# Kernel optimization log

Hardware: AMD Instinct MI355X
Metric: run time of the kernel (lower is better)

The kernel has to match this reference:

```python
import jax, jax.numpy as jnp
import numpy as np

D_MODEL = 1024
NUM_HEADS = 16
D_K = D_MODEL // NUM_HEADS


def setup_inputs() -> dict:
    key = jax.random.key(0)
    ks = jax.random.split(key, 11)
    B, S = 2, 2048
    scale = 1.0 / np.sqrt(D_MODEL)
    inp = {
        "q": jax.random.normal(ks[0], (B, S, D_MODEL), jnp.float32),
        "k": jax.random.normal(ks[1], (B, S, D_MODEL), jnp.float32),
        "v": jax.random.normal(ks[2], (B, S, D_MODEL), jnp.float32),
        "Wq": jax.random.normal(ks[3], (D_MODEL, D_MODEL), jnp.float32) * scale,
        "bq": jnp.zeros((D_MODEL,), jnp.float32),
        "Wk": jax.random.normal(ks[4], (D_MODEL, D_MODEL), jnp.float32) * scale,
        "bk": jnp.zeros((D_MODEL,), jnp.float32),
        "Wv": jax.random.normal(ks[5], (D_MODEL, D_MODEL), jnp.float32) * scale,
        "bv": jnp.zeros((D_MODEL,), jnp.float32),
        "Wo": jax.random.normal(ks[6], (D_MODEL, D_MODEL), jnp.float32) * scale,
        "bo": jnp.zeros((D_MODEL,), jnp.float32),
    }
    return inp


def _split_heads(x):
    B, S, _ = x.shape
    return x.reshape(B, S, NUM_HEADS, D_K).transpose(0, 2, 1, 3)  # [B,H,S,dk]


def reference(q, k, v, Wq, bq, Wk, bk, Wv, bv, Wo, bo):
    Q = _split_heads(q @ Wq.T + bq)  # [B,H,S,dk]
    K = _split_heads(k @ Wk.T + bk)
    V = _split_heads(v @ Wv.T + bv)
    scores = jnp.einsum("bhqd,bhkd->bhqk", Q, K) / jnp.sqrt(jnp.float32(D_K))
    attn = jax.nn.softmax(scores, axis=-1)
    ctx = jnp.einsum("bhqk,bhkd->bhqd", attn, V)  # [B,H,S,dk]
    B, H, S, dk = ctx.shape
    ctx = ctx.transpose(0, 2, 1, 3).reshape(B, S, D_MODEL)
    return ctx @ Wo.T + bo
```

## Files before the change

kernel.cpp:

```cpp
#include <hip/hip_runtime.h>
#include <hip/hip_bf16.h>

typedef unsigned short ushort_t;
typedef __attribute__((ext_vector_type(4))) float f32x4;
typedef __attribute__((ext_vector_type(16))) float f32x16;
typedef __attribute__((ext_vector_type(8))) short short8;
typedef __attribute__((ext_vector_type(4))) unsigned short us4;

#define D_MODEL 1024
#define NHEAD 16
#define DK 64
#define BATCH 2
#define SEQ 2048
#define MTOT 4096
#define EX (MTOT * D_MODEL)
#define EW (D_MODEL * D_MODEL)
#define NROWS (32 * SEQ)

#define MFMA16(a,b,c) __builtin_amdgcn_mfma_f32_16x16x32_bf16((a),(b),(c),0,0,0)
#define MFMA32(a,b,c) __builtin_amdgcn_mfma_f32_32x32x16_bf16((a),(b),(c),0,0,0)

__device__ __forceinline__ ushort_t f2bf(float f){
    union{float f;unsigned u;}c; c.f=f;
    unsigned u=c.u, r=u+0x7FFFu+((u>>16)&1u);
    return (ushort_t)(r>>16);
}
__device__ __forceinline__ unsigned cvtpk_bf(float a, float b){
    float2 t; t.x = a; t.y = b;
    union{ __hip_bfloat162 h; unsigned u; } c;
    c.h = __float22bfloat162_rn(t);
    return c.u;
}
__device__ __forceinline__ void plswap(unsigned &a, unsigned &b){
    asm volatile("v_permlane32_swap_b32 %0, %1" : "+v"(a), "+v"(b));
}
__device__ __forceinline__ void gload16(const ushort_t* g, ushort_t* l){
    __builtin_amdgcn_global_load_lds((const __attribute__((address_space(1))) unsigned*)g,
                                     (__attribute__((address_space(3))) unsigned*)l, 16, 0, 0);
}
__device__ __forceinline__ int xcd_swz(int nwg){
    int s = blockIdx.x;
    return (s & 7) * (nwg >> 3) + (s >> 3);
}

__global__ void cast1(const float* __restrict__ x, ushort_t* __restrict__ y, int n4){
    int i = blockIdx.x*blockDim.x + threadIdx.x, st = gridDim.x*blockDim.x;
    for(; i < n4; i += st){
        f32x4 v = ((const f32x4*)x)[i];
        us4 o; o[0]=f2bf(v[0]); o[1]=f2bf(v[1]); o[2]=f2bf(v[2]); o[3]=f2bf(v[3]);
        ((us4*)y)[i] = o;
    }
}
__global__ void cast4(const float* __restrict__ a, const float* __restrict__ b,
                      const float* __restrict__ c, const float* __restrict__ d4,
                      ushort_t* __restrict__ dst, int n4){
    const float* s = blockIdx.y==0 ? a : (blockIdx.y==1 ? b : (blockIdx.y==2 ? c : d4));
    us4* d = (us4*)(dst + (size_t)blockIdx.y * n4 * 4);
    const f32x4* sv = (const f32x4*)s;
    int i = blockIdx.x*blockDim.x + threadIdx.x, st = gridDim.x*blockDim.x;
    for(; i < n4; i += st){
        f32x4 v = sv[i];
        us4 o; o[0]=f2bf(v[0]); o[1]=f2bf(v[1]); o[2]=f2bf(v[2]); o[3]=f2bf(v[3]);
        d[i] = o;
    }
}

__device__ __forceinline__ void gemm_body(
    const ushort_t* __restrict__ A, const ushort_t* __restrict__ Bm,
    const float* __restrict__ bias, float scale, int bm, int bn, int mode,
    void* __restrict__ out,
    ushort_t* As0, ushort_t* As1, ushort_t* Bs0, ushort_t* Bs1)
{
    const int tid = threadIdx.x, lane = tid & 63, wid = tid >> 6;
    const int row0 = bm << 7, col0 = bn << 7;
    const int wrow = (wid >> 1) << 6, wcol = (wid & 1) << 6;
    const int l4 = lane >> 2, lc = (lane & 3) << 3, lr = lane & 15, ko = (lane >> 4) << 3;
    const f32x4 Z4 = {0.f,0.f,0.f,0.f};

    f32x4 acc[4][4];
#pragma unroll
    for(int i=0;i<4;i++)
#pragma unroll
        for(int j=0;j<4;j++) acc[i][j] = Z4;

#define GSTAGE(AS,BS,k0) do{ \
    gload16(A +(size_t)(row0+32*wid   +l4)*D_MODEL+(k0)+lc, (AS)+(2*wid  )*512); \
    gload16(A +(size_t)(row0+32*wid+16+l4)*D_MODEL+(k0)+lc, (AS)+(2*wid+1)*512); \
    gload16(Bm+(size_t)(col0+32*wid   +l4)*D_MODEL+(k0)+lc, (BS)+(2*wid  )*512); \
    gload16(Bm+(size_t)(col0+32*wid+16+l4)*D_MODEL+(k0)+lc, (BS)+(2*wid+1)*512); \
}while(0)
#define GCOMP(AS,BS) do{ \
    short8 af[4], bf[4]; \
    _Pragma("unroll") for(int i=0;i<4;i++) af[i]=*(const short8*)((AS)+(wrow+i*16+lr)*32+ko); \
    _Pragma("unroll") for(int j=0;j<4;j++) bf[j]=*(const short8*)((BS)+(wcol+j*16+lr)*32+ko); \
    __builtin_amdgcn_s_setprio(1); \
    _Pragma("unroll") for(int i=0;i<4;i++) \
    _Pragma("unroll") for(int j=0;j<4;j++) acc[i][j]=MFMA16(af[i],bf[j],acc[i][j]); \
    __builtin_amdgcn_s_setprio(0); \
}while(0)

    GSTAGE(As0,Bs0,0);
    __syncthreads();
#pragma unroll 1
    for(int t=0; t<32; t+=2){
        if(t+1<32) GSTAGE(As1,Bs1,(t+1)*32);
        GCOMP(As0,Bs0);
        __syncthreads();
        if(t+2<32) GSTAGE(As0,Bs0,(t+2)*32);
        GCOMP(As1,Bs1);
        __syncthreads();
    }
#undef GSTAGE

    const int rr4 = (lane >> 4) << 2;
#pragma unroll
    for(int i=0;i<4;i++){
#pragma unroll
        for(int j=0;j<4;j++){
            const int m0 = row0 + wrow + i*16 + rr4;
            const int n  = col0 + wcol + j*16 + lr;
            const float bs = bias[n];
            if(mode == 2){
                float* O = (float*)out;
#pragma unroll
                for(int r=0;r<4;r++) O[(size_t)(m0+r)*D_MODEL+n] = (acc[i][j][r]+bs)*scale;
            } else if(mode == 0){
                ushort_t* O = (ushort_t*)out;
#pragma unroll
                for(int r=0;r<4;r++) O[(size_t)(m0+r)*D_MODEL+n] = f2bf((acc[i][j][r]+bs)*scale);
            } else {
                ushort_t* O = (ushort_t*)out;
                const int bb = m0 >> 11, s = m0 & 2047, h = n >> 6, d = n & 63;
                us4 p;
#pragma unroll
                for(int r=0;r<4;r++) p[r] = f2bf((acc[i][j][r]+bs)*scale);
                *(us4*)(O + ((size_t)(bb*NHEAD + h)*DK + d)*SEQ + s) = p;
            }
        }
    }
#undef GCOMP
}

#define QSCALE (0.125f * 1.44269504088896f)

__global__ __launch_bounds__(256,2)
void qkv_fused(const float* __restrict__ Xq, const float* __restrict__ Xk,
               const float* __restrict__ Xv,
               const ushort_t* __restrict__ Wq, const ushort_t* __restrict__ Wk,
               const ushort_t* __restrict__ Wv,
               const float* __restrict__ bq, const float* __restrict__ bk,
               const float* __restrict__ bv,
               ushort_t* Qp, ushort_t* Kp, ushort_t* VtG)
{
    __shared__ ushort_t As0[4096], As1[4096], Bs0[4096], Bs1[4096];
    const int wk = xcd_swz(768);
    const int which = wk >> 8, t = wk & 255;
    const float *Af; const ushort_t *Bm; const float* bias; float scale; int mode; void* out;
    if(which == 0){ Af=Xq; Bm=Wq; bias=bq; scale=QSCALE; mode=0; out=Qp; }
    else if(which == 1){ Af=Xk; Bm=Wk; bias=bk; scale=1.f; mode=0; out=Kp; }
    else { Af=Xv; Bm=Wv; bias=bv; scale=1.f; mode=1; out=VtG; }

    const int bm = t >> 3, bn = t & 7;
    const int tid = threadIdx.x, lane = tid & 63, wid = tid >> 6;
    const int row0 = bm << 7, col0 = bn << 7;
    const int wrow = (wid >> 1) << 6, wcol = (wid & 1) << 6;
    const int l4 = lane >> 2, lc = (lane & 3) << 3, lr = lane & 15, ko = (lane >> 4) << 3;
    const f32x4 Z4 = {0.f,0.f,0.f,0.f};

    f32x4 acc[4][4];
#pragma unroll
    for(int i=0;i<4;i++)
#pragma unroll
        for(int j=0;j<4;j++) acc[i][j] = Z4;

    f32x4 ar[2][2][2];

#define ALOAD(R, k0) do{ \
    _Pragma("unroll") for(int c=0;c<2;c++){ \
        const float* src = Af + (size_t)(row0+32*wid+16*c+l4)*D_MODEL + (k0)+lc; \
        (R)[c][0] = *(const f32x4*)(src); \
        (R)[c][1] = *(const f32x4*)(src+4); \
    } \
}while(0)
#define AWRITE(AS, R) do{ \
    _Pragma("unroll") for(int c=0;c<2;c++){ \
        union{ unsigned u[4]; short8 s; } P; \
        P.u[0]=cvtpk_bf((R)[c][0][0],(R)[c][0][1]); \
        P.u[1]=cvtpk_bf((R)[c][0][2],(R)[c][0][3]); \
        P.u[2]=cvtpk_bf((R)[c][1][0],(R)[c][1][1]); \
        P.u[3]=cvtpk_bf((R)[c][1][2],(R)[c][1][3]); \
        *(short8*)((AS) + (2*wid+c)*512 + lane*8) = P.s; \
    } \
}while(0)
#define BSTAGE(BS,k0) do{ \
    gload16(Bm+(size_t)(col0+32*wid   +l4)*D_MODEL+(k0)+lc, (BS)+(2*wid  )*512); \
    gload16(Bm+(size_t)(col0+32*wid+16+l4)*D_MODEL+(k0)+lc, (BS)+(2*wid+1)*512); \
}while(0)
#define GCOMP(AS,BS) do{ \
    short8 af[4], bf[4]; \
    _Pragma("unroll") for(int i=0;i<4;i++) af[i]=*(const short8*)((AS)+(wrow+i*16+lr)*32+ko); \
    _Pragma("unroll") for(int j=0;j<4;j++) bf[j]=*(const short8*)((BS)+(wcol+j*16+lr)*32+ko); \
    __builtin_amdgcn_s_setprio(1); \
    _Pragma("unroll") for(int i=0;i<4;i++) \
    _Pragma("unroll") for(int j=0;j<4;j++) acc[i][j]=MFMA16(af[i],bf[j],acc[i][j]); \
    __builtin_amdgcn_s_setprio(0); \
}while(0)

    ALOAD(ar[0], 0); BSTAGE(Bs0, 0);
    AWRITE(As0, ar[0]);
    __syncthreads();
#pragma unroll 1
    for(int t2=0; t2<32; t2+=2){
        if(t2+1<32){ ALOAD(ar[1], (t2+1)*32); BSTAGE(Bs1, (t2+1)*32); }
        GCOMP(As0,Bs0);
        if(t2+1<32) AWRITE(As1, ar[1]);
        __syncthreads();
        if(t2+2<32){ ALOAD(ar[0], (t2+2)*32); BSTAGE(Bs0, (t2+2)*32); }
        GCOMP(As1,Bs1);
        if(t2+2<32) AWRITE(As0, ar[0]);
        __syncthreads();
    }
#undef ALOAD
#undef AWRITE
#undef BSTAGE
#undef GCOMP

    const int rr4 = (lane >> 4) << 2;
#pragma unroll
    for(int i=0;i<4;i++){
#pragma unroll
        for(int j=0;j<4;j++){
            const int m0 = row0 + wrow + i*16 + rr4;
            const int n  = col0 + wcol + j*16 + lr;
            const float bs = bias[n];
            if(mode == 0){
                ushort_t* O = (ushort_t*)out;
#pragma unroll
                for(int r=0;r<4;r++) O[(size_t)(m0+r)*D_MODEL+n] = f2bf((acc[i][j][r]+bs)*scale);
            } else {
                ushort_t* O = (ushort_t*)out;
                const int bb = m0 >> 11, s = m0 & 2047, h = n >> 6, d = n & 63;
                us4 p;
#pragma unroll
                for(int r=0;r<4;r++) p[r] = f2bf((acc[i][j][r]+bs)*scale);
                *(us4*)(O + ((size_t)(bb*NHEAD + h)*DK + d)*SEQ + s) = p;
            }
        }
    }
}

__global__ __launch_bounds__(256,2)
void gemm_one(const ushort_t* __restrict__ A, const ushort_t* __restrict__ Bm,
              const float* __restrict__ bias, float scale, int mode, void* out)
{
    __shared__ ushort_t As0[4096], As1[4096], Bs0[4096], Bs1[4096];
    const int wk = xcd_swz(256);
    gemm_body(A,Bm,bias,scale, wk>>3, wk&7, mode, out, As0,As1,Bs0,Bs1);
}

__global__ __launch_bounds__(128,2)
void attn_fwd(const ushort_t* __restrict__ Qp, const ushort_t* __restrict__ Kp,
              const ushort_t* __restrict__ VtG, ushort_t* __restrict__ ctx)
{
    __shared__ ushort_t Ks0[64*64], Ks1[64*64];
    __shared__ ushort_t Vs0[64*64], Vs1[64*64];

    const int wk = xcd_swz(1024);
    const int bh = wk >> 5, qt = wk & 31;
    const int b = bh >> 4, h = bh & 15;
    const int tid = threadIdx.x, lane = tid & 63, wid = tid >> 6;
    const int lq = lane & 31, hi = lane >> 5, lx = lq & 7;
    const size_t qkbase = (size_t)b*SEQ*D_MODEL + h*DK;
    const size_t vbase  = (size_t)bh * DK * SEQ;
    const int q0 = qt*64 + wid*32;

    short8 qa[4];
#pragma unroll
    for(int s=0;s<4;s++)
        qa[s] = *(const short8*)(Qp + qkbase + (size_t)(q0+lq)*D_MODEL + s*16 + hi*8);

    f32x16 o[2];
    float run_m = -1e30f, run_l = 0.f;
#pragma unroll
    for(int i=0;i<16;i++){ o[0][i] = 0.f; o[1][i] = 0.f; }

    const int srow = lane >> 3;
    const int jsw  = (((lane & 7) ^ srow) << 3);

#define ASTAGE(KS, VS, kv) do{ \
    _Pragma("unroll") for(int c=0;c<4;c++){ \
        const int rb = wid*32 + c*8; \
        gload16(Kp  + qkbase + (size_t)((kv)+rb+srow)*D_MODEL + jsw, (KS) + rb*64); \
        gload16(VtG + vbase  + (size_t)(rb+srow)*SEQ + (kv) + jsw,   (VS) + rb*64); \
    } \
}while(0)

#define APHASE(KS, VS) do{ \
    f32x16 st0, st1; \
    __builtin_amdgcn_s_setprio(1); \
    { f32x16 acc; \
      _Pragma("unroll") for(int i=0;i<16;i++) acc[i]=0.f; \
      _Pragma("unroll") for(int s=0;s<4;s++){ \
          short8 kf = *(const short8*)((KS) + lq*64 + (((2*s+hi)^lx)<<3)); \
          acc = MFMA32(kf, qa[s], acc); } \
      st0 = acc; } \
    { f32x16 acc; \
      _Pragma("unroll") for(int i=0;i<16;i++) acc[i]=0.f; \
      _Pragma("unroll") for(int s=0;s<4;s++){ \
          short8 kf = *(const short8*)((KS) + (32+lq)*64 + (((2*s+hi)^lx)<<3)); \
          acc = MFMA32(kf, qa[s], acc); } \
      st1 = acc; } \
    __builtin_amdgcn_s_setprio(0); \
    float tr[8]; \
    _Pragma("unroll") for(int i=0;i<8;i++) tr[i] = fmaxf(fmaxf(st0[i],st0[i+8]), fmaxf(st1[i],st1[i+8])); \
    _Pragma("unroll") for(int w=4;w;w>>=1) \
    _Pragma("unroll") for(int i=0;i<w;i++) tr[i]=fmaxf(tr[i],tr[i+w]); \
    const float pmax = fmaxf(tr[0], __shfl_xor(tr[0], 32)); \
    if(__any(pmax > run_m + 8.f)){ \
        const float nm = fmaxf(run_m, pmax); \
        const float corr = exp2f(run_m - nm); \
        run_m = nm; run_l *= corr; \
        _Pragma("unroll") for(int i=0;i<16;i++){ o[0][i]*=corr; o[1][i]*=corr; } \
    } \
    float ts[16]; \
    _Pragma("unroll") for(int i=0;i<16;i++){ \
        st0[i] = exp2f(st0[i] - run_m); \
        st1[i] = exp2f(st1[i] - run_m); \
        ts[i] = st0[i] + st1[i]; } \
    _Pragma("unroll") for(int w=8;w;w>>=1) \
    _Pragma("unroll") for(int i=0;i<w;i++) ts[i]+=ts[i+w]; \
    run_l += ts[0] + __shfl_xor(ts[0], 32); \
    _Pragma("unroll") for(int sub=0; sub<2; sub++){ \
        unsigned w8[8]; \
        _Pragma("unroll") for(int i=0;i<8;i++) \
            w8[i] = cvtpk_bf(sub==0 ? st0[2*i] : st1[2*i], sub==0 ? st0[2*i+1] : st1[2*i+1]); \
        plswap(w8[0], w8[2]); plswap(w8[1], w8[3]); \
        plswap(w8[4], w8[6]); plswap(w8[5], w8[7]); \
        union { unsigned u[4]; short8 s; } p0, p1; \
        p0.u[0]=w8[0]; p0.u[1]=w8[1]; p0.u[2]=w8[2]; p0.u[3]=w8[3]; \
        p1.u[0]=w8[4]; p1.u[1]=w8[5]; p1.u[2]=w8[6]; p1.u[3]=w8[7]; \
        __builtin_amdgcn_s_setprio(1); \
        _Pragma("unroll") for(int ds=0; ds<2; ds++){ \
            short8 v0 = *(const short8*)((VS) + (ds*32+lq)*64 + (((sub*4+0+hi)^lx)<<3)); \
            short8 v1 = *(const short8*)((VS) + (ds*32+lq)*64 + (((sub*4+2+hi)^lx)<<3)); \
            o[ds] = MFMA32(v0, p0.s, o[ds]); \
            o[ds] = MFMA32(v1, p1.s, o[ds]); } \
        __builtin_amdgcn_s_setprio(0); \
    } \
}while(0)

    ASTAGE(Ks0, Vs0, 0);
    __syncthreads();
#pragma unroll 1
    for(int kv0 = 0; kv0 < SEQ; kv0 += 128){
        if(kv0 + 64 < SEQ) ASTAGE(Ks1, Vs1, kv0 + 64);
        APHASE(Ks0, Vs0);
        __syncthreads();
        if(kv0 + 128 < SEQ) ASTAGE(Ks0, Vs0, kv0 + 128);
        APHASE(Ks1, Vs1);
        __syncthreads();
    }
#undef ASTAGE

    const float linv = 1.f / run_l;
#pragma unroll
    for(int ds=0; ds<2; ds++)
#pragma unroll
        for(int g=0; g<4; g++){
            unsigned lo = cvtpk_bf(o[ds][4*g+0]*linv, o[ds][4*g+1]*linv);
            unsigned hi2 = cvtpk_bf(o[ds][4*g+2]*linv, o[ds][4*g+3]*linv);
            union { unsigned u[2]; us4 v; } pp; pp.u[0]=lo; pp.u[1]=hi2;
            *(us4*)(ctx + qkbase + (size_t)(q0+lq)*D_MODEL + ds*32 + 8*g + 4*hi) = pp.v;
        }
}

__global__ __launch_bounds__(128,4)
void attn_split(const ushort_t* __restrict__ Qp, const ushort_t* __restrict__ Kp,
                const ushort_t* __restrict__ VtG,
                float* __restrict__ Op, float* __restrict__ Lp)
{
    __shared__ ushort_t Ks[64*64];
    __shared__ ushort_t Vs[64*64];

    const int wk = xcd_swz(2048);
    const int half = wk & 1, bhqt = wk >> 1;
    const int bh = bhqt >> 5, qt = bhqt & 31;
    const int b = bh >> 4, h = bh & 15;
    const int tid = threadIdx.x, lane = tid & 63, wid = tid >> 6;
    const int lq = lane & 31, hi = lane >> 5, lx = lq & 7;
    const size_t qkbase = (size_t)b*SEQ*D_MODEL + h*DK;
    const size_t vbase  = (size_t)bh * DK * SEQ;
    const int q0 = qt*64 + wid*32;
    const int kvbeg = half * (SEQ/2);

    short8 qa[4];
#pragma unroll
    for(int s=0;s<4;s++)
        qa[s] = *(const short8*)(Qp + qkbase + (size_t)(q0+lq)*D_MODEL + s*16 + hi*8);

    const f32x16 Z16 = {0.f,0.f,0.f,0.f,0.f,0.f,0.f,0.f,0.f,0.f,0.f,0.f,0.f,0.f,0.f,0.f};
    f32x16 o[2];
    float2 run_l2; run_l2.x = 0.f; run_l2.y = 0.f;
    o[0] = Z16; o[1] = Z16;

    const int srow = lane >> 3;
    const int jsw  = (((lane & 7) ^ srow) << 3);

#pragma unroll 1
    for(int kv0 = kvbeg; kv0 < kvbeg + SEQ/2; kv0 += 64){
#pragma unroll
        for(int c=0;c<4;c++){
            const int rb = wid*32 + c*8;
            gload16(Kp  + qkbase + (size_t)(kv0+rb+srow)*D_MODEL + jsw, Ks + rb*64);
            gload16(VtG + vbase  + (size_t)(rb+srow)*SEQ + kv0 + jsw,   Vs + rb*64);
        }
        __syncthreads();

        f32x16 st0, st1;
        __builtin_amdgcn_s_setprio(1);
        {
            f32x16 acc = Z16;
#pragma unroll
            for(int s=0;s<4;s++){
                short8 kf = *(const short8*)(Ks + lq*64 + (((2*s+hi)^lx)<<3));
                acc = MFMA32(kf, qa[s], acc);
            }
            st0 = acc;
        }
        {
            f32x16 acc = Z16;
#pragma unroll
            for(int s=0;s<4;s++){
                short8 kf = *(const short8*)(Ks + (32+lq)*64 + (((2*s+hi)^lx)<<3));
                acc = MFMA32(kf, qa[s], acc);
            }
            st1 = acc;
        }
        __builtin_amdgcn_s_setprio(0);

#pragma unroll
        for(int i=0;i<16;i++){
            st0[i] = exp2f(st0[i]);
            st1[i] = exp2f(st1[i]);
        }
        float2 t2[8];
#pragma unroll
        for(int i=0;i<8;i++){
            t2[i].x = st0[2*i] + st1[2*i];
            t2[i].y = st0[2*i+1] + st1[2*i+1];
        }
#pragma unroll
        for(int w=4;w;w>>=1)
#pragma unroll
            for(int i=0;i<w;i++){ t2[i].x += t2[i+w].x; t2[i].y += t2[i+w].y; }
        run_l2.x += t2[0].x; run_l2.y += t2[0].y;

#pragma unroll
        for(int sub=0; sub<2; sub++){
            unsigned w8[8];
#pragma unroll
            for(int i=0;i<8;i++)
                w8[i] = cvtpk_bf(sub==0 ? st0[2*i] : st1[2*i], sub==0 ? st0[2*i+1] : st1[2*i+1]);
            plswap(w8[0], w8[2]); plswap(w8[1], w8[3]);
            plswap(w8[4], w8[6]); plswap(w8[5], w8[7]);
            union { unsigned u[4]; short8 s; } p0, p1;
            p0.u[0]=w8[0]; p0.u[1]=w8[1]; p0.u[2]=w8[2]; p0.u[3]=w8[3];
            p1.u[0]=w8[4]; p1.u[1]=w8[5]; p1.u[2]=w8[6]; p1.u[3]=w8[7];
            __builtin_amdgcn_s_setprio(1);
#pragma unroll
            for(int ds=0; ds<2; ds++){
                short8 v0 = *(const short8*)(Vs + (ds*32+lq)*64 + (((sub*4+0+hi)^lx)<<3));
                short8 v1 = *(const short8*)(Vs + (ds*32+lq)*64 + (((sub*4+2+hi)^lx)<<3));
                o[ds] = MFMA32(v0, p0.s, o[ds]);
                o[ds] = MFMA32(v1, p1.s, o[ds]);
            }
            __builtin_amdgcn_s_setprio(0);
        }
        __syncthreads();
    }

    float lsum = run_l2.x + run_l2.y;
    lsum += __shfl_xor(lsum, 32);

    const size_t rbase = ((size_t)half*NROWS + (size_t)bh*SEQ + q0 + lq) * 64;
#pragma unroll
    for(int ds=0; ds<2; ds++)
#pragma unroll
        for(int g=0; g<4; g++){
            f32x4 v; v[0]=o[ds][4*g+0]; v[1]=o[ds][4*g+1]; v[2]=o[ds][4*g+2]; v[3]=o[ds][4*g+3];
            *(f32x4*)(Op + rbase + ds*32 + 8*g + 4*hi) = v;
        }
    if(hi == 0)
        Lp[(size_t)half*NROWS + (size_t)bh*SEQ + q0 + lq] = lsum;
}

__global__ void attn_combine(const float* __restrict__ Op, const float* __restrict__ Lp,
                             ushort_t* __restrict__ ctx)
{
    const int lane = threadIdx.x & 63;
    int w = blockIdx.x * (blockDim.x >> 6) + (threadIdx.x >> 6);
    const int nw = gridDim.x * (blockDim.x >> 6);
    for(int row = w; row < NROWS; row += nw){
        float inv = 1.f / (Lp[row] + Lp[NROWS + row]);
        float o0 = Op[(size_t)row*64 + lane];
        float o1 = Op[((size_t)NROWS + row)*64 + lane];
        float o = (o0 + o1) * inv;
        const int bh = row >> 11, q = row & 2047;
        const int b = bh >> 4, h = bh & 15;
        ctx[((size_t)b*SEQ + q)*D_MODEL + h*DK + lane] = f2bf(o);
    }
}

extern "C" void kernel_launch(void* const* d_in, const int* in_sizes, int n_in,
                              void* d_out, int out_size, void* d_ws, size_t ws_size,
                              hipStream_t stream) {
    (void)in_sizes; (void)n_in; (void)out_size;
    const float* q  = (const float*)d_in[0];
    const float* k  = (const float*)d_in[1];
    const float* v  = (const float*)d_in[2];
    const float* Wq = (const float*)d_in[3];
    const float* bq = (const float*)d_in[4];
    const float* Wk = (const float*)d_in[5];
    const float* bk = (const float*)d_in[6];
    const float* Wv = (const float*)d_in[7];
    const float* bv = (const float*)d_in[8];
    const float* Wo = (const float*)d_in[9];
    const float* bo = (const float*)d_in[10];
    float* out = (float*)d_out;

    ushort_t* WS = (ushort_t*)d_ws;
    const dim3 blk(256);
    const int n4x = EX/4, n4w = EW/4;

    const size_t tierA2 = ((size_t)4*EW + (size_t)4*EX) * 2
                        + ((size_t)2*NROWS*64 + (size_t)2*NROWS) * 4;
    const size_t tierA1 = ((size_t)4*EW + (size_t)4*EX) * 2;

    if(ws_size >= tierA1){
        ushort_t* Wqb = WS;
        ushort_t* Wkb = Wqb + EW;
        ushort_t* Wvb = Wkb + EW;
        ushort_t* Wob = Wvb + EW;
        ushort_t* Qp  = Wob + EW;
        ushort_t* Kp  = Qp + EX;
        ushort_t* VtG = Kp + EX;
        ushort_t* ctx = VtG + EX;

        cast4<<<dim3(256,4), blk, 0, stream>>>(Wq, Wk, Wv, Wo, Wqb, n4w);
        qkv_fused<<<768, blk, 0, stream>>>(q, k, v, Wqb, Wkb, Wvb, bq, bk, bv, Qp, Kp, VtG);

        if(ws_size >= tierA2){
            float* Op = (float*)(ctx + EX);
            float* Lp = Op + (size_t)2*NROWS*64;
            attn_split<<<2048, dim3(128), 0, stream>>>(Qp, Kp, VtG, Op, Lp);
            attn_combine<<<2048, blk, 0, stream>>>(Op, Lp, ctx);
        } else {
            attn_fwd<<<1024, dim3(128), 0, stream>>>(Qp, Kp, VtG, ctx);
        }
        gemm_one<<<256, blk, 0, stream>>>(ctx, Wob, bo, 1.f, 2, out);
    } else {
        ushort_t* Xb  = WS;
        ushort_t* Wb  = Xb + EX;
        ushort_t* Qp  = Wb + EW;
        ushort_t* Kp  = Qp + EX;
        ushort_t* VtG = Kp + EX;
        ushort_t* ctx = Xb;

        cast1<<<1024, blk, 0, stream>>>(q, Xb, n4x);
        cast1<<<512,  blk, 0, stream>>>(Wq, Wb, n4w);
        gemm_one<<<256, blk, 0, stream>>>(Xb, Wb, bq, QSCALE, 0, Qp);
        cast1<<<1024, blk, 0, stream>>>(k, Xb, n4x);
        cast1<<<512,  blk, 0, stream>>>(Wk, Wb, n4w);
        gemm_one<<<256, blk, 0, stream>>>(Xb, Wb, bk, 1.f, 0, Kp);
        cast1<<<1024, blk, 0, stream>>>(v, Xb, n4x);
        cast1<<<512,  blk, 0, stream>>>(Wv, Wb, n4w);
        gemm_one<<<256, blk, 0, stream>>>(Xb, Wb, bv, 1.f, 1, VtG);
        attn_fwd<<<1024, dim3(128), 0, stream>>>(Qp, Kp, VtG, ctx);
        cast1<<<512, blk, 0, stream>>>(Wo, Wb, n4w);
        gemm_one<<<256, blk, 0, stream>>>(ctx, Wb, bo, 1.f, 2, out);
    }
}
```

Before: 142.3 us.

## Fuse split-KV attention halves into one block with LDS combine

Replaces the two-kernel split-KV attention (attn_split writing fp32 partials to global, then attn_combine) with a single 256-thread kernel. Two of its waves process the first half of the keys and the other two process the second half, and the halves are merged through shared memory before the bf16 context is written. This removes the global round trip of fp32 partial outputs and one kernel launch. In exchange each block now needs 32KB of LDS and a larger block, which may reduce occupancy.

After: 130.6 us. 1.09x faster.

```diff
diff --git a/kernel.cpp b/kernel.cpp
--- a/kernel.cpp
+++ b/kernel.cpp
@@ -15,7 +15,6 @@
 #define MTOT 4096
 #define EX (MTOT * D_MODEL)
 #define EW (D_MODEL * D_MODEL)
-#define NROWS (32 * SEQ)
 
 #define MFMA16(a,b,c) __builtin_amdgcn_mfma_f32_16x16x32_bf16((a),(b),(c),0,0,0)
 #define MFMA32(a,b,c) __builtin_amdgcn_mfma_f32_32x32x16_bf16((a),(b),(c),0,0,0)
@@ -256,6 +255,143 @@
     __shared__ ushort_t As0[4096], As1[4096], Bs0[4096], Bs1[4096];
     const int wk = xcd_swz(256);
     gemm_body(A,Bm,bias,scale, wk>>3, wk&7, mode, out, As0,As1,Bs0,Bs1);
+}
+
+__global__ __launch_bounds__(256,4)
+void attn_half(const ushort_t* __restrict__ Qp, const ushort_t* __restrict__ Kp,
+               const ushort_t* __restrict__ VtG, ushort_t* __restrict__ ctx)
+{
+    __shared__ ushort_t KV[4][64*64];
+
+    const int wk = xcd_swz(1024);
+    const int bh = wk >> 5, qt = wk & 31;
+    const int b = bh >> 4, h = bh & 15;
+    const int tid = threadIdx.x, lane = tid & 63, wid = tid >> 6;
+    const int qgrp = wid & 1, half = wid >> 1;
+    const int lq = lane & 31, hi = lane >> 5, lx = lq & 7;
+    const size_t qkbase = (size_t)b*SEQ*D_MODEL + h*DK;
+    const size_t vbase  = (size_t)bh * DK * SEQ;
+    const int q0 = qt*64 + qgrp*32;
+    const int kvbase = half * (SEQ/2);
+
+    ushort_t* Ksb = KV[half*2];
+    ushort_t* Vsb = KV[half*2+1];
+
+    short8 qa[4];
+#pragma unroll
+    for(int s=0;s<4;s++)
+        qa[s] = *(const short8*)(Qp + qkbase + (size_t)(q0+lq)*D_MODEL + s*16 + hi*8);
+
+    const f32x16 Z16 = {0.f,0.f,0.f,0.f,0.f,0.f,0.f,0.f,0.f,0.f,0.f,0.f,0.f,0.f,0.f,0.f};
+    f32x16 o[2];
+    float2 run_l2; run_l2.x = 0.f; run_l2.y = 0.f;
+    o[0] = Z16; o[1] = Z16;
+
+    const int srow = lane >> 3;
+    const int jsw  = (((lane & 7) ^ srow) << 3);
+
+#pragma unroll 1
+    for(int kv0 = 0; kv0 < SEQ/2; kv0 += 64){
+#pragma unroll
+        for(int c=0;c<4;c++){
+            const int rb = qgrp*32 + c*8;
+            gload16(Kp  + qkbase + (size_t)(kvbase+kv0+rb+srow)*D_MODEL + jsw, Ksb + rb*64);
+            gload16(VtG + vbase  + (size_t)(rb+srow)*SEQ + kvbase+kv0 + jsw,   Vsb + rb*64);
+        }
+        __syncthreads();
+
+        f32x16 st0, st1;
+        __builtin_amdgcn_s_setprio(1);
+        {
+            f32x16 acc = Z16;
+#pragma unroll
+            for(int s=0;s<4;s++){
+                short8 kf = *(const short8*)(Ksb + lq*64 + (((2*s+hi)^lx)<<3));
+                acc = MFMA32(kf, qa[s], acc);
+            }
+            st0 = acc;
+        }
+        {
+            f32x16 acc = Z16;
+#pragma unroll
+            for(int s=0;s<4;s++){
+                short8 kf = *(const short8*)(Ksb + (32+lq)*64 + (((2*s+hi)^lx)<<3));
+                acc = MFMA32(kf, qa[s], acc);
+            }
+            st1 = acc;
+        }
+        __builtin_amdgcn_s_setprio(0);
+
+#pragma unroll
+        for(int i=0;i<16;i++){
+            st0[i] = exp2f(st0[i]);
+            st1[i] = exp2f(st1[i]);
+        }
+        float2 t2[8];
+#pragma unroll
+        for(int i=0;i<8;i++){
+            t2[i].x = st0[2*i] + st1[2*i];
+            t2[i].y = st0[2*i+1] + st1[2*i+1];
+        }
+#pragma unroll
+        for(int w=4;w;w>>=1)
+#pragma unroll
+            for(int i=0;i<w;i++){ t2[i].x += t2[i+w].x; t2[i].y += t2[i+w].y; }
+        run_l2.x += t2[0].x; run_l2.y += t2[0].y;
+
+#pragma unroll
+        for(int sub=0; sub<2; sub++){
+            unsigned w8[8];
+#pragma unroll
+            for(int i=0;i<8;i++)
+                w8[i] = cvtpk_bf(sub==0 ? st0[2*i] : st1[2*i], sub==0 ? st0[2*i+1] : st1[2*i+1]);
+            plswap(w8[0], w8[2]); plswap(w8[1], w8[3]);
+            plswap(w8[4], w8[6]); plswap(w8[5], w8[7]);
+            union { unsigned u[4]; short8 s; } p0, p1;
+            p0.u[0]=w8[0]; p0.u[1]=w8[1]; p0.u[2]=w8[2]; p0.u[3]=w8[3];
+            p1.u[0]=w8[4]; p1.u[1]=w8[5]; p1.u[2]=w8[6]; p1.u[3]=w8[7];
+            __builtin_amdgcn_s_setprio(1);
+#pragma unroll
+            for(int ds=0; ds<2; ds++){
+                short8 v0 = *(const short8*)(Vsb + (ds*32+lq)*64 + (((sub*4+0+hi)^lx)<<3));
+                short8 v1 = *(const short8*)(Vsb + (ds*32+lq)*64 + (((sub*4+2+hi)^lx)<<3));
+                o[ds] = MFMA32(v0, p0.s, o[ds]);
+                o[ds] = MFMA32(v1, p1.s, o[ds]);
+            }
+            __builtin_amdgcn_s_setprio(0);
+        }
+        __syncthreads();
+    }
+
+    float lsum = run_l2.x + run_l2.y;
+    lsum += __shfl_xor(lsum, 32);
+
+    float* Xo = (float*)&KV[0][0];
+    float* Xl = Xo + 64*68;
+    if(half == 1){
+#pragma unroll
+        for(int ds=0; ds<2; ds++)
+#pragma unroll
+            for(int g=0; g<4; g++){
+                f32x4 v; v[0]=o[ds][4*g+0]; v[1]=o[ds][4*g+1]; v[2]=o[ds][4*g+2]; v[3]=o[ds][4*g+3];
+                *(f32x4*)(Xo + (qgrp*32+lq)*68 + ds*32 + 8*g + 4*hi) = v;
+            }
+        if(hi == 0) Xl[qgrp*32+lq] = lsum;
+    }
+    __syncthreads();
+    if(half == 0){
+        const float inv = 1.f / (lsum + Xl[qgrp*32+lq]);
+#pragma unroll
+        for(int ds=0; ds<2; ds++)
+#pragma unroll
+            for(int g=0; g<4; g++){
+                f32x4 oo = *(const f32x4*)(Xo + (qgrp*32+lq)*68 + ds*32 + 8*g + 4*hi);
+                unsigned lo  = cvtpk_bf((o[ds][4*g+0]+oo[0])*inv, (o[ds][4*g+1]+oo[1])*inv);
+                unsigned hi2 = cvtpk_bf((o[ds][4*g+2]+oo[2])*inv, (o[ds][4*g+3]+oo[3])*inv);
+                union { unsigned u[2]; us4 v; } pp; pp.u[0]=lo; pp.u[1]=hi2;
+                *(us4*)(ctx + qkbase + (size_t)(q0+lq)*D_MODEL + ds*32 + 8*g + 4*hi) = pp.v;
+            }
+    }
 }
 
 __global__ __launch_bounds__(128,2)
@@ -374,143 +510,6 @@
         }
 }
 
-__global__ __launch_bounds__(128,4)
-void attn_split(const ushort_t* __restrict__ Qp, const ushort_t* __restrict__ Kp,
-                const ushort_t* __restrict__ VtG,
-                float* __restrict__ Op, float* __restrict__ Lp)
-{
-    __shared__ ushort_t Ks[64*64];
-    __shared__ ushort_t Vs[64*64];
-
-    const int wk = xcd_swz(2048);
-    const int half = wk & 1, bhqt = wk >> 1;
-    const int bh = bhqt >> 5, qt = bhqt & 31;
-    const int b = bh >> 4, h = bh & 15;
-    const int tid = threadIdx.x, lane = tid & 63, wid = tid >> 6;
-    const int lq = lane & 31, hi = lane >> 5, lx = lq & 7;
-    const size_t qkbase = (size_t)b*SEQ*D_MODEL + h*DK;
-    const size_t vbase  = (size_t)bh * DK * SEQ;
-    const int q0 = qt*64 + wid*32;
-    const int kvbeg = half * (SEQ/2);
-
-    short8 qa[4];
-#pragma unroll
-    for(int s=0;s<4;s++)
-        qa[s] = *(const short8*)(Qp + qkbase + (size_t)(q0+lq)*D_MODEL + s*16 + hi*8);
-
-    const f32x16 Z16 = {0.f,0.f,0.f,0.f,0.f,0.f,0.f,0.f,0.f,0.f,0.f,0.f,0.f,0.f,0.f,0.f};
-    f32x16 o[2];
-    float2 run_l2; run_l2.x = 0.f; run_l2.y = 0.f;
-    o[0] = Z16; o[1] = Z16;
-
-    const int srow = lane >> 3;
-    const int jsw  = (((lane & 7) ^ srow) << 3);
-
-#pragma unroll 1
-    for(int kv0 = kvbeg; kv0 < kvbeg + SEQ/2; kv0 += 64){
-#pragma unroll
-        for(int c=0;c<4;c++){
-            const int rb = wid*32 + c*8;
-            gload16(Kp  + qkbase + (size_t)(kv0+rb+srow)*D_MODEL + jsw, Ks + rb*64);
-            gload16(VtG + vbase  + (size_t)(rb+srow)*SEQ + kv0 + jsw,   Vs + rb*64);
-        }
-        __syncthreads();
-
-        f32x16 st0, st1;
-        __builtin_amdgcn_s_setprio(1);
-        {
-            f32x16 acc = Z16;
-#pragma unroll
-            for(int s=0;s<4;s++){
-                short8 kf = *(const short8*)(Ks + lq*64 + (((2*s+hi)^lx)<<3));
-                acc = MFMA32(kf, qa[s], acc);
-            }
-            st0 = acc;
-        }
-        {
-            f32x16 acc = Z16;
-#pragma unroll
-            for(int s=0;s<4;s++){
-                short8 kf = *(const short8*)(Ks + (32+lq)*64 + (((2*s+hi)^lx)<<3));
-                acc = MFMA32(kf, qa[s], acc);
-            }
-            st1 = acc;
-        }
-        __builtin_amdgcn_s_setprio(0);
-
-#pragma unroll
-        for(int i=0;i<16;i++){
-            st0[i] = exp2f(st0[i]);
-            st1[i] = exp2f(st1[i]);
-        }
-        float2 t2[8];
-#pragma unroll
-        for(int i=0;i<8;i++){
-            t2[i].x = st0[2*i] + st1[2*i];
-            t2[i].y = st0[2*i+1] + st1[2*i+1];
-        }
-#pragma unroll
-        for(int w=4;w;w>>=1)
-#pragma unroll
-            for(int i=0;i<w;i++){ t2[i].x += t2[i+w].x; t2[i].y += t2[i+w].y; }
-        run_l2.x += t2[0].x; run_l2.y += t2[0].y;
-
-#pragma unroll
-        for(int sub=0; sub<2; sub++){
-            unsigned w8[8];
-#pragma unroll
-            for(int i=0;i<8;i++)
-                w8[i] = cvtpk_bf(sub==0 ? st0[2*i] : st1[2*i], sub==0 ? st0[2*i+1] : st1[2*i+1]);
-            plswap(w8[0], w8[2]); plswap(w8[1], w8[3]);
-            plswap(w8[4], w8[6]); plswap(w8[5], w8[7]);
-            union { unsigned u[4]; short8 s; } p0, p1;
-            p0.u[0]=w8[0]; p0.u[1]=w8[1]; p0.u[2]=w8[2]; p0.u[3]=w8[3];
-            p1.u[0]=w8[4]; p1.u[1]=w8[5]; p1.u[2]=w8[6]; p1.u[3]=w8[7];
-            __builtin_amdgcn_s_setprio(1);
-#pragma unroll
-            for(int ds=0; ds<2; ds++){
-                short8 v0 = *(const short8*)(Vs + (ds*32+lq)*64 + (((sub*4+0+hi)^lx)<<3));
-                short8 v1 = *(const short8*)(Vs + (ds*32+lq)*64 + (((sub*4+2+hi)^lx)<<3));
-                o[ds] = MFMA32(v0, p0.s, o[ds]);
-                o[ds] = MFMA32(v1, p1.s, o[ds]);
-            }
-            __builtin_amdgcn_s_setprio(0);
-        }
-        __syncthreads();
-    }
-
-    float lsum = run_l2.x + run_l2.y;
-    lsum += __shfl_xor(lsum, 32);
-
-    const size_t rbase = ((size_t)half*NROWS + (size_t)bh*SEQ + q0 + lq) * 64;
-#pragma unroll
-    for(int ds=0; ds<2; ds++)
-#pragma unroll
-        for(int g=0; g<4; g++){
-            f32x4 v; v[0]=o[ds][4*g+0]; v[1]=o[ds][4*g+1]; v[2]=o[ds][4*g+2]; v[3]=o[ds][4*g+3];
-            *(f32x4*)(Op + rbase + ds*32 + 8*g + 4*hi) = v;
-        }
-    if(hi == 0)
-        Lp[(size_t)half*NROWS + (size_t)bh*SEQ + q0 + lq] = lsum;
-}
-
-__global__ void attn_combine(const float* __restrict__ Op, const float* __restrict__ Lp,
-                             ushort_t* __restrict__ ctx)
-{
-    const int lane = threadIdx.x & 63;
-    int w = blockIdx.x * (blockDim.x >> 6) + (threadIdx.x >> 6);
-    const int nw = gridDim.x * (blockDim.x >> 6);
-    for(int row = w; row < NROWS; row += nw){
-        float inv = 1.f / (Lp[row] + Lp[NROWS + row]);
-        float o0 = Op[(size_t)row*64 + lane];
-        float o1 = Op[((size_t)NROWS + row)*64 + lane];
-        float o = (o0 + o1) * inv;
-        const int bh = row >> 11, q = row & 2047;
-        const int b = bh >> 4, h = bh & 15;
-        ctx[((size_t)b*SEQ + q)*D_MODEL + h*DK + lane] = f2bf(o);
-    }
-}
-
 extern "C" void kernel_launch(void* const* d_in, const int* in_sizes, int n_in,
                               void* d_out, int out_size, void* d_ws, size_t ws_size,
                               hipStream_t stream) {
@@ -532,11 +531,9 @@
     const dim3 blk(256);
     const int n4x = EX/4, n4w = EW/4;
 
-    const size_t tierA2 = ((size_t)4*EW + (size_t)4*EX) * 2
-                        + ((size_t)2*NROWS*64 + (size_t)2*NROWS) * 4;
-    const size_t tierA1 = ((size_t)4*EW + (size_t)4*EX) * 2;
-
-    if(ws_size >= tierA1){
+    const size_t tierA = ((size_t)4*EW + (size_t)4*EX) * 2;
+
+    if(ws_size >= tierA){
         ushort_t* Wqb = WS;
         ushort_t* Wkb = Wqb + EW;
         ushort_t* Wvb = Wkb + EW;
@@ -548,15 +545,7 @@
 
         cast4<<<dim3(256,4), blk, 0, stream>>>(Wq, Wk, Wv, Wo, Wqb, n4w);
         qkv_fused<<<768, blk, 0, stream>>>(q, k, v, Wqb, Wkb, Wvb, bq, bk, bv, Qp, Kp, VtG);
-
-        if(ws_size >= tierA2){
-            float* Op = (float*)(ctx + EX);
-            float* Lp = Op + (size_t)2*NROWS*64;
-            attn_split<<<2048, dim3(128), 0, stream>>>(Qp, Kp, VtG, Op, Lp);
-            attn_combine<<<2048, blk, 0, stream>>>(Op, Lp, ctx);
-        } else {
-            attn_fwd<<<1024, dim3(128), 0, stream>>>(Qp, Kp, VtG, ctx);
-        }
+        attn_half<<<1024, blk, 0, stream>>>(Qp, Kp, VtG, ctx);
         gemm_one<<<256, blk, 0, stream>>>(ctx, Wob, bo, 1.f, 2, out);
     } else {
         ushort_t* Xb  = WS;
```
